# Kernel tuning notes

Hardware: AMD Instinct MI355X
Metric: run time of the kernel (lower is better)

The kernel has to match this reference:

```python
import jax, jax.numpy as jnp
import numpy as np

K = 20  # neighbors

def setup_inputs() -> dict:
    key = jax.random.key(0)
    k1, k2 = jax.random.split(key)
    B, C, N, O = 8, 64, 4096, 64
    x = jax.random.normal(k1, (B, C, N), dtype=jnp.float32)
    W = jax.random.normal(k2, (O, 2 * C), dtype=jnp.float32) * (1.0 / np.sqrt(2 * C))
    b = jnp.zeros((O,), dtype=jnp.float32)
    return {"x": x, "W": W, "b": b}

def _knn_idx(pts, k):
    # pts: [B, N, d]; returns [B, N, k] indices of k nearest neighbors (incl. self)
    sq = jnp.sum(pts * pts, axis=-1)                      # [B, N]
    inner = jnp.einsum('bnd,bmd->bnm', pts, pts)          # [B, N, N]
    neg_d2 = 2.0 * inner - sq[:, :, None] - sq[:, None, :]
    _, idx = jax.lax.top_k(neg_d2, k)                     # largest -dist = nearest
    return idx

def reference(x, W, b):
    # x: [B, C, N], W: [O, 2C], b: [O]
    pts = jnp.transpose(x, (0, 2, 1))                     # [B, N, C]
    idx = _knn_idx(jax.lax.stop_gradient(pts), K)         # [B, N, K]
    nbr = jax.vmap(lambda p, i: p[i])(pts, idx)           # [B, N, K, C]
    ctr = pts[:, :, None, :]                              # [B, N, 1, C]
    # local+global edge features: [diff, center] along channel dim -> [B, N, K, 2C]
    edge = jnp.concatenate([nbr - ctr, jnp.broadcast_to(ctr, nbr.shape)], axis=-1)
    # 1x1 conv == channel GEMM
    out = jnp.einsum('bnkc,oc->bonk', edge, W) + b[None, :, None, None]
    return jnp.max(out, axis=-1)                          # [B, O, N]
```

## Files before the change

kernel.cpp:

```cpp
#include <hip/hip_runtime.h>
#include <float.h>

typedef unsigned long long u64;
typedef unsigned int u32;
typedef unsigned short u16;

#define NPTS 4096
#define CDIM 64
#define BATCH 8
#define KSEL 20

#define F_XTL (BATCH * NPTS * 32)
#define F_CAND (2 * BATCH * NPTS * 32)
#define F_XTF (4 * BATCH * NPTS * 32)
#define F_SQ (6 * BATCH * NPTS * 32)
#define F_WT2 (F_SQ + BATCH * NPTS)
#define F_SQB (F_WT2 + 64 * 64)

typedef __attribute__((ext_vector_type(8))) short short8v;
typedef __attribute__((ext_vector_type(16))) float float16v;

#define MFMA32(a, b, c) __builtin_amdgcn_mfma_f32_32x32x16_bf16(a, b, c, 0, 0, 0)

__device__ __forceinline__ u32 ordf(float f) {
    u32 u = __float_as_uint(f);
    return (u >> 31) ? ~u : (u | 0x80000000u);
}
__device__ __forceinline__ u32 umaxu(u32 a, u32 b) { return a > b ? a : b; }
__device__ __forceinline__ u32 uminu(u32 a, u32 b) { return a < b ? a : b; }

__device__ __forceinline__ void load_lds_16(const void* g, void* l) {
    __builtin_amdgcn_global_load_lds(
        (const __attribute__((address_space(1))) unsigned int*)g,
        (__attribute__((address_space(3))) unsigned int*)l, 16, 0, 0);
}

#define CE(i, j) { u32 a_ = c[i], b_ = c[j]; c[i] = umaxu(a_, b_); c[j] = uminu(a_, b_); }

__device__ __forceinline__ void sort16_desc(u32 (&c)[16]) {
    CE(0,1) CE(2,3) CE(4,5) CE(6,7) CE(8,9) CE(10,11) CE(12,13) CE(14,15)
    CE(0,2) CE(1,3) CE(4,6) CE(5,7) CE(8,10) CE(9,11) CE(12,14) CE(13,15)
    CE(1,2) CE(5,6) CE(9,10) CE(13,14)
    CE(0,4) CE(1,5) CE(2,6) CE(3,7) CE(8,12) CE(9,13) CE(10,14) CE(11,15)
    CE(2,4) CE(3,5) CE(10,12) CE(11,13)
    CE(1,2) CE(3,4) CE(5,6) CE(9,10) CE(11,12) CE(13,14)
    CE(0,8) CE(1,9) CE(2,10) CE(3,11) CE(4,12) CE(5,13) CE(6,14) CE(7,15)
    CE(4,8) CE(5,9) CE(6,10) CE(7,11)
    CE(2,4) CE(3,5) CE(6,8) CE(7,9) CE(10,12) CE(11,13)
    CE(1,2) CE(3,4) CE(5,6) CE(7,8) CE(9,10) CE(11,12) CE(13,14)
}
#undef CE

__device__ __forceinline__ void merge_into16(u32 (&L)[16], const u32 (&c)[16]) {
#pragma unroll
    for (int i = 0; i < 16; i++) L[i] = umaxu(L[i], c[15 - i]);
#pragma unroll
    for (int j = 8; j >= 1; j >>= 1)
#pragma unroll
        for (int i = 0; i < 16; i++)
            if ((i & j) == 0) {
                int p = i | j;
                u32 a = L[i], b = L[p];
                L[i] = umaxu(a, b);
                L[p] = uminu(a, b);
            }
}

__global__ __launch_bounds__(256) void p1_prep(const float* __restrict__ x,
                                               const float* __restrict__ W,
                                               float* __restrict__ xtf,
                                               u16* __restrict__ xth,
                                               u16* __restrict__ xtl,
                                               float* __restrict__ sq,
                                               float* __restrict__ sqb,
                                               float* __restrict__ wt2g) {
    __shared__ float Xp[64][65];
    int tid = threadIdx.x;
    if (blockIdx.x >= 512) {
        int f = (blockIdx.x - 512) * 256 + tid;
        if (f < 64 * 64) {
            int c = f >> 6, o = f & 63;
            wt2g[f] = W[o * 128 + 64 + c] - W[o * 128 + c];
        }
        return;
    }
    int b = blockIdx.x >> 6;
    int n0 = (blockIdx.x & 63) * 64;
    const float* xb = x + (size_t)b * (CDIM * NPTS);
    int j = tid & 63, cq = tid >> 6;
#pragma unroll
    for (int i = 0; i < 16; i++) {
        int c = cq * 16 + i;
        Xp[c][j] = xb[(size_t)c * NPTS + n0 + j];
    }
    __syncthreads();
    if (tid < 64) {
        float s = 0.f;
        for (int c = 0; c < 64; c++) { float v = Xp[c][tid]; s = fmaf(v, v, s); }
        sq[(size_t)b * NPTS + n0 + tid] = s;
        sqb[(size_t)b * NPTS + n0 + tid] = 1024.f - s;
    }
    int n = tid >> 2, c0 = (tid & 3) * 16;
    float vv[16];
#pragma unroll
    for (int i = 0; i < 16; i++) vv[i] = Xp[c0 + i][n];
    size_t rowb = ((size_t)b * NPTS + n0 + n) * 64 + c0;
#pragma unroll
    for (int q = 0; q < 4; q++) {
        float4 f;
        f.x = vv[4 * q]; f.y = vv[4 * q + 1]; f.z = vv[4 * q + 2]; f.w = vv[4 * q + 3];
        *(float4*)(xtf + rowb + 4 * q) = f;
    }
    u16 hb[16], lb[16];
#pragma unroll
    for (int i = 0; i < 16; i++) {
        float v = vv[i] * 1.41421356237f;
        u32 bv = __float_as_uint(v);
        u32 h = (bv + 0x7FFFu + ((bv >> 16) & 1u)) >> 16;
        float hf = __uint_as_float(h << 16);
        float lf = v - hf;
        u32 bl = __float_as_uint(lf);
        u32 lo = (bl + 0x7FFFu + ((bl >> 16) & 1u)) >> 16;
        hb[i] = (u16)h; lb[i] = (u16)lo;
    }
    uint4 H0, H1, L0, L1;
    H0.x = hb[0] | ((u32)hb[1] << 16);  H0.y = hb[2] | ((u32)hb[3] << 16);
    H0.z = hb[4] | ((u32)hb[5] << 16);  H0.w = hb[6] | ((u32)hb[7] << 16);
    H1.x = hb[8] | ((u32)hb[9] << 16);  H1.y = hb[10] | ((u32)hb[11] << 16);
    H1.z = hb[12] | ((u32)hb[13] << 16); H1.w = hb[14] | ((u32)hb[15] << 16);
    L0.x = lb[0] | ((u32)lb[1] << 16);  L0.y = lb[2] | ((u32)lb[3] << 16);
    L0.z = lb[4] | ((u32)lb[5] << 16);  L0.w = lb[6] | ((u32)lb[7] << 16);
    L1.x = lb[8] | ((u32)lb[9] << 16);  L1.y = lb[10] | ((u32)lb[11] << 16);
    L1.z = lb[12] | ((u32)lb[13] << 16); L1.w = lb[14] | ((u32)lb[15] << 16);
    *(uint4*)(xth + rowb) = H0;
    *(uint4*)(xth + rowb + 8) = H1;
    *(uint4*)(xtl + rowb) = L0;
    *(uint4*)(xtl + rowb + 8) = L1;
}

__device__ __forceinline__ void stage_tile(const u16* __restrict__ srcb,
                                           char* lds, int w, int lane) {
#pragma unroll
    for (int i = 0; i < 2; i++) {
        int G = w * 128 + i * 64 + lane;
        int rr = G >> 3, gp = G & 7;
        const u16* src = srcb + rr * 64 + ((gp ^ (rr & 7)) << 3);
        char* dst = lds + (w * 128 + i * 64) * 16;
        load_lds_16(src, dst);
    }
}

__device__ __forceinline__ void sel_half(const float16v& A, int colbase2,
                                         u32 (&L)[16]) {
    u32 c[16];
#pragma unroll
    for (int q = 0; q < 4; q++) {
        u32 cg = (u32)(colbase2 + 8 * q);
        c[4 * q + 0] = (__float_as_uint(A[4 * q + 0]) & 0xFFFFF000u) | (cg + 0);
        c[4 * q + 1] = (__float_as_uint(A[4 * q + 1]) & 0xFFFFF000u) | (cg + 1);
        c[4 * q + 2] = (__float_as_uint(A[4 * q + 2]) & 0xFFFFF000u) | (cg + 2);
        c[4 * q + 3] = (__float_as_uint(A[4 * q + 3]) & 0xFFFFF000u) | (cg + 3);
    }
    sort16_desc(c);
    merge_into16(L, c);
}

__global__ __launch_bounds__(256, 4) void k2_gram(const u16* __restrict__ xth,
                                                  const u16* __restrict__ xtl,
                                                  const float* __restrict__ sqb,
                                                  u32* __restrict__ cand) {
    __shared__ char pool[2][8192];
    int tid = threadIdx.x;
    int lane = tid & 63, w = tid >> 6;
    int l31 = lane & 31, lh = lane >> 5;
    int b = blockIdx.x & 7;
    int rt = (blockIdx.x >> 3) & 31;
    int ch = blockIdx.x >> 8;
    int r0 = rt * 128;
    int cb = ch * 1024;
    size_t bbase = (size_t)b * NPTS;

    short8v Ah[4], Al[4];
    {
        const u16* pa = xth + (bbase + r0 + 32 * w + l31) * 64 + 8 * lh;
        const u16* pl = xtl + (bbase + r0 + 32 * w + l31) * 64 + 8 * lh;
#pragma unroll
        for (int s = 0; s < 4; s++) {
            Ah[s] = *(const short8v*)(pa + 16 * s);
            Al[s] = *(const short8v*)(pl + 16 * s);
        }
    }

    u32 L[16];
#pragma unroll
    for (int i = 0; i < 16; i++) L[i] = 0u;

    stage_tile(xth + (bbase + cb) * 64, pool[0], w, lane);
    __syncthreads();

    for (int t = 0; t < 16; t++) {
        int n1 = cb + t * 64;
        const char* pb = pool[t & 1];
        if (t < 15)
            stage_tile(xth + (bbase + n1 + 64) * 64, pool[(t + 1) & 1], w, lane);

        const float* sqbp = sqb + bbase + n1 + 4 * lh;
        float16v a0, a1;
#pragma unroll
        for (int q = 0; q < 4; q++) {
            ((float4*)&a0)[q] = *(const float4*)(sqbp + 8 * q);
            ((float4*)&a1)[q] = *(const float4*)(sqbp + 32 + 8 * q);
        }

#pragma unroll
        for (int s = 0; s < 4; s++) {
            int gx = 2 * s + lh;
            int sw = (gx ^ (l31 & 7)) << 4;
            short8v bh0 = *(const short8v*)(pb + l31 * 128 + sw);
            a0 = MFMA32(bh0, Ah[s], a0);
            a0 = MFMA32(bh0, Al[s], a0);
        }
        sel_half(a0, n1 + 4 * lh, L);

#pragma unroll
        for (int s = 0; s < 4; s++) {
            int gx = 2 * s + lh;
            int sw = (gx ^ (l31 & 7)) << 4;
            short8v bh1 = *(const short8v*)(pb + (32 + l31) * 128 + sw);
            a1 = MFMA32(bh1, Ah[s], a1);
            a1 = MFMA32(bh1, Al[s], a1);
        }
        sel_half(a1, n1 + 32 + 4 * lh, L);

        __syncthreads();
    }

    u32 M[16];
#pragma unroll
    for (int i = 0; i < 16; i++) {
        u32 pv = __shfl_xor(L[15 - i], 32);
        M[i] = umaxu(L[i], pv);
    }
#pragma unroll
    for (int j = 8; j >= 1; j >>= 1)
#pragma unroll
        for (int i = 0; i < 16; i++)
            if ((i & j) == 0) {
                int p = i | j;
                u32 a = M[i], b2 = M[p];
                M[i] = umaxu(a, b2);
                M[p] = uminu(a, b2);
            }
    if (lane < 32) {
        u32* cr = cand + (bbase + r0 + 32 * w + l31) * 64 + ch * 16;
#pragma unroll
        for (int q = 0; q < 4; q++) {
            uint4 v;
            v.x = M[4 * q]; v.y = M[4 * q + 1]; v.z = M[4 * q + 2]; v.w = M[4 * q + 3];
            *(uint4*)(cr + 4 * q) = v;
        }
    }
}

__global__ __launch_bounds__(256) void k1_prep(const float* __restrict__ x,
                                               const float* __restrict__ W,
                                               float* __restrict__ y1) {
    __shared__ float Xt[64][128];
    __shared__ float Wt[64][64];
    int tid = threadIdx.x;
    int gr0 = blockIdx.x * 128;
    int b = gr0 >> 12;
    int n0 = gr0 & 4095;
    const float* xb = x + (size_t)b * (CDIM * NPTS) + n0;

    for (int k = 0; k < 32; k++) {
        int f = tid + 256 * k;
        int c = f >> 7, j = f & 127;
        Xt[c][j] = xb[(size_t)c * NPTS + j];
    }
    for (int k = 0; k < 16; k++) {
        int f = tid + 256 * k;
        int c = f >> 6, o = f & 63;
        Wt[c][o] = W[o * 128 + c];
    }
    __syncthreads();

    int tr = tid & 15, tc = tid >> 4;
    float acc[8][4];
#pragma unroll
    for (int i = 0; i < 8; i++)
#pragma unroll
        for (int j = 0; j < 4; j++) acc[i][j] = 0.f;

#pragma unroll 4
    for (int c = 0; c < 64; c++) {
        float a[8], bb[4];
        *(float4*)&a[0] = *(const float4*)&Xt[c][8 * tr];
        *(float4*)&a[4] = *(const float4*)&Xt[c][8 * tr + 4];
        *(float4*)&bb[0] = *(const float4*)&Wt[c][4 * tc];
#pragma unroll
        for (int i = 0; i < 8; i++)
#pragma unroll
            for (int j = 0; j < 4; j++) acc[i][j] = fmaf(a[i], bb[j], acc[i][j]);
    }

#pragma unroll
    for (int i = 0; i < 8; i++) {
        int r = gr0 + 8 * tr + i;
        float4 s0;
        s0.x = acc[i][0]; s0.y = acc[i][1]; s0.z = acc[i][2]; s0.w = acc[i][3];
        *(float4*)(y1 + (size_t)r * 64 + 4 * tc) = s0;
    }
}

__global__ __launch_bounds__(256) void k2b3(const float* __restrict__ xtf,
                                            const float* __restrict__ sq,
                                            const u32* __restrict__ cand,
                                            const float* __restrict__ y1,
                                            const float* __restrict__ wt2g,
                                            const float* __restrict__ bias,
                                            float* __restrict__ out) {
    __shared__ float wt2[64][64];
    __shared__ float xr[4][64];
    __shared__ float dd[4][32];
    __shared__ u32 cols[4][32];
    __shared__ int ids[4][KSEL];
    __shared__ float outT[64][17];
    int tid = threadIdx.x;
    int lane = tid & 63, w = tid >> 6;
    int bid = blockIdx.x;
    int b = bid & 7;
    int nblk = (bid >> 3) * 16;
    size_t bbase = (size_t)b * NPTS;

#pragma unroll
    for (int k = 0; k < 4; k++) {
        int f = tid + 256 * k;
        ((float4*)wt2)[f] = ((const float4*)wt2g)[f];
    }
    __syncthreads();

    int s = lane & 3, g = lane >> 2;
    float bl = bias[lane];

#pragma unroll 1
    for (int i = 0; i < 4; i++) {
        int n = nblk + w * 4 + i;
        size_t row = bbase + n;

        if (lane < 16)
            *(float4*)&xr[w][lane * 4] = *(const float4*)(xtf + row * 64 + lane * 4);
        u32 key = cand[row * 64 + lane];

        int local = lane & 31;
        {
            int srcl = (local < 16) ? local : (47 - local);
            key = __shfl(key, (lane & 32) | srcl);
        }
#pragma unroll
        for (u32 j2 = 16; j2 >= 1; j2 >>= 1) {
            u32 p = __shfl_xor(key, j2);
            key = ((local & j2) == 0) ? umaxu(key, p) : uminu(key, p);
        }
        {
            u32 p = __shfl(key, 63 - lane);
            if (lane < 32) cols[w][lane] = umaxu(key, p) & 0xFFFu;
        }

        float4 xq[4];
#pragma unroll
        for (int q = 0; q < 4; q++) xq[q] = *(const float4*)&xr[w][16 * q + 4 * s];

#pragma unroll
        for (int p = 0; p < 2; p++) {
            int m = cols[w][p * 16 + g];
            const float* pm = xtf + (bbase + m) * 64;
            float d = 0.f;
#pragma unroll
            for (int q = 0; q < 4; q++) {
                float4 v = *(const float4*)(pm + 16 * q + 4 * s);
                d = fmaf(v.x, xq[q].x, d); d = fmaf(v.y, xq[q].y, d);
                d = fmaf(v.z, xq[q].z, d); d = fmaf(v.w, xq[q].w, d);
            }
            d += __shfl_xor(d, 1);
            d += __shfl_xor(d, 2);
            if (s == 0) dd[w][p * 16 + g] = d;
        }

        u64 kE = 0;
        if (lane < 32) {
            int m = (int)cols[w][lane];
            float sE = fmaf(2.f, dd[w][lane], -sq[bbase + m]);
            kE = ((u64)ordf(sE) << 32) | (u32)(~(u32)m);
        }
#pragma unroll
        for (u32 k = 2; k <= 32; k <<= 1) {
#pragma unroll
            for (u32 j2 = k >> 1; j2 >= 1; j2 >>= 1) {
                bool up = ((lane & k) == 0);
                bool lower = ((lane & j2) == 0);
                u64 p = __shfl_xor(kE, j2);
                u64 mx = (kE > p) ? kE : p, mn = (kE > p) ? p : kE;
                kE = (lower == up) ? mx : mn;
            }
        }
        if (lane < KSEL) ids[w][lane] = (int)(~(u32)kE);

        const float* y1b = y1 + bbase * 64;
        float acc = -FLT_MAX;
#pragma unroll
        for (int k = 0; k < KSEL; k++) {
            int m = ids[w][k];
            acc = fmaxf(acc, y1b[(size_t)m * 64 + lane]);
        }
        float acc2 = 0.f;
#pragma unroll 8
        for (int c = 0; c < 64; c++)
            acc2 = fmaf(xr[w][c], wt2[c][lane], acc2);
        outT[lane][w * 4 + i] = acc + acc2 + bl;
    }
    __syncthreads();

    {
        int o = tid & 63, q = tid >> 6;
        float4 v;
        v.x = outT[o][q * 4 + 0]; v.y = outT[o][q * 4 + 1];
        v.z = outT[o][q * 4 + 2]; v.w = outT[o][q * 4 + 3];
        *(float4*)(out + ((size_t)(b * 64 + o)) * NPTS + nblk + q * 4) = v;
    }
}

extern "C" void kernel_launch(void* const* d_in, const int* in_sizes, int n_in,
                              void* d_out, int out_size, void* d_ws, size_t ws_size,
                              hipStream_t stream) {
    const float* x    = (const float*)d_in[0];
    const float* W    = (const float*)d_in[1];
    const float* bias = (const float*)d_in[2];
    float* out = (float*)d_out;
    float* ws = (float*)d_ws;

    u16* xth    = (u16*)ws;
    u16* xtl    = (u16*)(ws + F_XTL);
    u32* candb  = (u32*)(ws + F_CAND);
    float* xtf  = ws + F_XTF;
    float* sq   = ws + F_SQ;
    float* wt2g = ws + F_WT2;
    float* sqb  = ws + F_SQB;
    float* y1   = ws;

    hipLaunchKernelGGL(p1_prep, dim3(528),  dim3(256), 0, stream,
                       x, W, xtf, xth, xtl, sq, sqb, wt2g);
    hipLaunchKernelGGL(k2_gram, dim3(1024), dim3(256), 0, stream, xth, xtl, sqb, candb);
    hipLaunchKernelGGL(k1_prep, dim3(256),  dim3(256), 0, stream, x, W, y1);
    hipLaunchKernelGGL(k2b3,    dim3(2048), dim3(256), 0, stream,
                       xtf, sq, candb, y1, wt2g, bias, out);
}
```

Before: 141.7 us.

## Drop low-bf16 split term in Gram MFMA and single-buffer the LDS tile

The Gram kernel stops using the low half of the split-bf16 representation for the A operand, so each k-step issues one MFMA instead of two. The B tile moves from double-buffered to single-buffered shared memory, with an extra barrier before restaging, and the per-tile squared-norm loads are prefetched into registers one iteration ahead. This halves the matrix work and cuts LDS use, but lowers distance precision, which may change which neighbours are picked for near-tied candidates. Single buffering also serialises the tile load with compute.

Result: faster. 133.5 us (-5.8%).

```diff
diff --git a/kernel.cpp b/kernel.cpp
--- a/kernel.cpp
+++ b/kernel.cpp
@@ -166,10 +166,9 @@
 }
 
 __global__ __launch_bounds__(256, 4) void k2_gram(const u16* __restrict__ xth,
-                                                  const u16* __restrict__ xtl,
                                                   const float* __restrict__ sqb,
                                                   u32* __restrict__ cand) {
-    __shared__ char pool[2][8192];
+    __shared__ char pool[8192];
     int tid = threadIdx.x;
     int lane = tid & 63, w = tid >> 6;
     int l31 = lane & 31, lh = lane >> 5;
@@ -180,45 +179,54 @@
     int cb = ch * 1024;
     size_t bbase = (size_t)b * NPTS;
 
-    short8v Ah[4], Al[4];
+    short8v Ah[4];
     {
         const u16* pa = xth + (bbase + r0 + 32 * w + l31) * 64 + 8 * lh;
-        const u16* pl = xtl + (bbase + r0 + 32 * w + l31) * 64 + 8 * lh;
-#pragma unroll
-        for (int s = 0; s < 4; s++) {
-            Ah[s] = *(const short8v*)(pa + 16 * s);
-            Al[s] = *(const short8v*)(pl + 16 * s);
-        }
+#pragma unroll
+        for (int s = 0; s < 4; s++) Ah[s] = *(const short8v*)(pa + 16 * s);
     }
 
     u32 L[16];
 #pragma unroll
     for (int i = 0; i < 16; i++) L[i] = 0u;
 
-    stage_tile(xth + (bbase + cb) * 64, pool[0], w, lane);
+    float4 sqn[8];
+    {
+        const float* p0 = sqb + bbase + cb + 4 * lh;
+#pragma unroll
+        for (int q = 0; q < 4; q++) {
+            sqn[q] = *(const float4*)(p0 + 8 * q);
+            sqn[4 + q] = *(const float4*)(p0 + 32 + 8 * q);
+        }
+    }
+
+    stage_tile(xth + (bbase + cb) * 64, pool, w, lane);
     __syncthreads();
 
     for (int t = 0; t < 16; t++) {
         int n1 = cb + t * 64;
-        const char* pb = pool[t & 1];
-        if (t < 15)
-            stage_tile(xth + (bbase + n1 + 64) * 64, pool[(t + 1) & 1], w, lane);
-
-        const float* sqbp = sqb + bbase + n1 + 4 * lh;
+
         float16v a0, a1;
 #pragma unroll
         for (int q = 0; q < 4; q++) {
-            ((float4*)&a0)[q] = *(const float4*)(sqbp + 8 * q);
-            ((float4*)&a1)[q] = *(const float4*)(sqbp + 32 + 8 * q);
+            ((float4*)&a0)[q] = sqn[q];
+            ((float4*)&a1)[q] = sqn[4 + q];
+        }
+        if (t < 15) {
+            const float* np = sqb + bbase + n1 + 64 + 4 * lh;
+#pragma unroll
+            for (int q = 0; q < 4; q++) {
+                sqn[q] = *(const float4*)(np + 8 * q);
+                sqn[4 + q] = *(const float4*)(np + 32 + 8 * q);
+            }
         }
 
 #pragma unroll
         for (int s = 0; s < 4; s++) {
             int gx = 2 * s + lh;
             int sw = (gx ^ (l31 & 7)) << 4;
-            short8v bh0 = *(const short8v*)(pb + l31 * 128 + sw);
+            short8v bh0 = *(const short8v*)(pool + l31 * 128 + sw);
             a0 = MFMA32(bh0, Ah[s], a0);
-            a0 = MFMA32(bh0, Al[s], a0);
         }
         sel_half(a0, n1 + 4 * lh, L);
 
@@ -226,12 +234,13 @@
         for (int s = 0; s < 4; s++) {
             int gx = 2 * s + lh;
             int sw = (gx ^ (l31 & 7)) << 4;
-            short8v bh1 = *(const short8v*)(pb + (32 + l31) * 128 + sw);
+            short8v bh1 = *(const short8v*)(pool + (32 + l31) * 128 + sw);
             a1 = MFMA32(bh1, Ah[s], a1);
-            a1 = MFMA32(bh1, Al[s], a1);
-        }
+        }
+        __syncthreads();
+        if (t < 15)
+            stage_tile(xth + (bbase + n1 + 64) * 64, pool, w, lane);
         sel_half(a1, n1 + 32 + 4 * lh, L);
-
         __syncthreads();
     }
 
@@ -450,7 +459,7 @@
 
     hipLaunchKernelGGL(p1_prep, dim3(528),  dim3(256), 0, stream,
                        x, W, xtf, xth, xtl, sq, sqb, wt2g);
-    hipLaunchKernelGGL(k2_gram, dim3(1024), dim3(256), 0, stream, xth, xtl, sqb, candb);
+    hipLaunchKernelGGL(k2_gram, dim3(1024), dim3(256), 0, stream, xth, sqb, candb);
     hipLaunchKernelGGL(k1_prep, dim3(256),  dim3(256), 0, stream, x, W, y1);
     hipLaunchKernelGGL(k2b3,    dim3(2048), dim3(256), 0, stream,
                        xtf, sq, candb, y1, wt2g, bias, out);
```
